# Kernel tuning notes

Hardware: AMD Instinct MI355X
Metric: run time of the kernel (lower is better)

The kernel has to match this reference:

```python
import jax, jax.numpy as jnp
import numpy as np

MAX_NODES = 1024
FEAT = 64
HID = 32
B, S = 32, 4096


def setup_inputs() -> dict:
    key = jax.random.key(0)
    ks = jax.random.split(key, 9)
    flow_features = jax.random.normal(ks[0], (B, S, FEAT), dtype=jnp.float32)
    src_ips = jax.random.randint(ks[1], (B, S), 0, MAX_NODES, dtype=jnp.int32)
    dst_ips = jax.random.randint(ks[2], (B, S), 0, MAX_NODES, dtype=jnp.int32)
    flow_volumes = jax.random.uniform(ks[3], (B, S), dtype=jnp.float32)
    # learned parameters
    node_emb = jax.random.normal(ks[4], (MAX_NODES, FEAT), dtype=jnp.float32)
    W1 = jax.random.normal(ks[5], (2 * FEAT, HID), dtype=jnp.float32) * (1.0 / np.sqrt(2 * FEAT))
    b1 = jnp.zeros((HID,), dtype=jnp.float32)
    W2 = jax.random.normal(ks[6], (HID, 1), dtype=jnp.float32) * (1.0 / np.sqrt(HID))
    b2 = jnp.zeros((1,), dtype=jnp.float32)
    return {"flow_features": flow_features, "src_ips": src_ips, "dst_ips": dst_ips,
            "flow_volumes": flow_volumes, "node_emb": node_emb,
            "W1": W1, "b1": b1, "W2": W2, "b2": b2}


def reference(flow_features, src_ips, dst_ips, flow_volumes, node_emb, W1, b1, W2, b2):
    b_, s_, f_ = flow_features.shape
    n_ = node_emb.shape[0]
    bidx = jnp.arange(b_)[:, None]  # (B,1) broadcast over seq

    # ---- scatter-add flow features into destination nodes ----
    node_features = jnp.zeros((b_, n_, f_), dtype=flow_features.dtype)
    node_features = node_features.at[bidx, dst_ips].add(flow_features)
    # F.normalize(p=2, dim=-1): x / max(||x||, eps)
    norm = jnp.linalg.norm(node_features, axis=-1, keepdims=True)
    node_features = node_features / jnp.maximum(norm, 1e-12)

    # ---- gather embeddings, edge MLP, scatter weights into adjacency ----
    src_e = node_emb[src_ips]  # (B,S,F)
    dst_e = node_emb[dst_ips]  # (B,S,F)
    h = jax.nn.relu(jnp.concatenate([src_e, dst_e], axis=-1) @ W1 + b1)  # (B,S,32)
    edge_w = jax.nn.sigmoid((h @ W2 + b2)[..., 0])  # (B,S)
    vol_w = jax.nn.sigmoid(flow_volumes / 1000.0)
    w = edge_w * vol_w  # (B,S)

    adjacency = jnp.zeros((b_, n_, n_), dtype=flow_features.dtype)
    # semantics up to scatter ordering of colliding edges)
    adjacency = adjacency.at[bidx, src_ips, dst_ips].set(w)
    adjacency = adjacency.at[bidx, dst_ips, src_ips].set(w)
    return node_features, adjacency
```

## Files before the change

kernel.cpp:

```cpp
#include <hip/hip_runtime.h>
#include <cstdint>
#include <cstddef>

#define BB 32
#define SS 4096
#define FEAT_ 64
#define HID_ 32
#define NN 1024

__global__ void node_feat_kernel(const float* __restrict__ flow,
                                 const int* __restrict__ dst,
                                 float* __restrict__ nf) {
    int row0 = blockIdx.x << 2;
    int b = row0 >> 10;
    __shared__ int sdst[SS];

    const int4* g = (const int4*)(dst + (size_t)b * SS);
    int4* sd4 = (int4*)sdst;
    for (int i = threadIdx.x; i < SS / 4; i += 256) sd4[i] = g[i];
    __syncthreads();

    int wave = threadIdx.x >> 6;
    int lane = threadIdx.x & 63;
    int node = (row0 + wave) & (NN - 1);
    const float* fb = flow + ((size_t)b * SS << 6);

    float acc = 0.0f;
    for (int s0 = 0; s0 < SS; s0 += 64) {
        int d = sdst[s0 + lane];
        unsigned long long m = __ballot(d == node);
        while (m) {
            int bit = __ffsll((long long)m) - 1;
            m &= m - 1;
            acc += fb[((s0 + bit) << 6) + lane];
        }
    }

    float ss = acc * acc;
    #pragma unroll
    for (int off = 32; off > 0; off >>= 1) ss += __shfl_xor(ss, off, 64);
    float denom = fmaxf(sqrtf(ss), 1e-12f);
    nf[((size_t)(row0 + wave) << 6) + lane] = acc / denom;
}

__global__ void scatter_prio_kernel(const int* __restrict__ src,
                                    const int* __restrict__ dst,
                                    float* __restrict__ adj) {
    int i = blockIdx.x * blockDim.x + threadIdx.x;
    int s = i & (SS - 1);
    int b = i >> 12;
    int si = src[i], di = dst[i];
    int* base = (int*)(adj + (size_t)b * NN * NN);
    atomicMax(base + si * NN + di, __float_as_int((float)(s + 1)));
    atomicMax(base + di * NN + si, __float_as_int((float)(SS + s + 1)));
}

__global__ void mlp_write_kernel(const int* __restrict__ src,
                                 const int* __restrict__ dst,
                                 const float* __restrict__ vol,
                                 const float* __restrict__ emb,
                                 const float* __restrict__ W1,
                                 const float* __restrict__ b1,
                                 const float* __restrict__ W2,
                                 const float* __restrict__ b2,
                                 float* __restrict__ adj) {
    int i = blockIdx.x * blockDim.x + threadIdx.x;
    int s = i & (SS - 1);
    int b = i >> 12;
    int si = src[i], di = dst[i];

    float acc[HID_];
    #pragma unroll
    for (int j = 0; j < HID_; ++j) acc[j] = b1[j];

    #pragma unroll
    for (int half = 0; half < 2; ++half) {
        const float* e = emb + ((half ? di : si) << 6);
        const float* w = W1 + half * 64 * HID_;
        for (int k = 0; k < 64; k += 4) {
            float4 v = *(const float4*)(e + k);
            #pragma unroll
            for (int j = 0; j < HID_; ++j) {
                float a = acc[j];
                a += v.x * w[(k + 0) * HID_ + j];
                a += v.y * w[(k + 1) * HID_ + j];
                a += v.z * w[(k + 2) * HID_ + j];
                a += v.w * w[(k + 3) * HID_ + j];
                acc[j] = a;
            }
        }
    }

    float dotv = b2[0];
    #pragma unroll
    for (int j = 0; j < HID_; ++j) dotv += fmaxf(acc[j], 0.0f) * W2[j];
    float edge_w = 1.0f / (1.0f + expf(-dotv));
    float vol_w  = 1.0f / (1.0f + expf(-vol[i] / 1000.0f));
    float wv = edge_w * vol_w;

    float* base = adj + (size_t)b * NN * NN;
    float* c1 = base + si * NN + di;
    float* c2 = base + di * NN + si;
    unsigned p1 = __float_as_uint((float)(s + 1));
    unsigned p2 = __float_as_uint((float)(SS + s + 1));
    if (__float_as_uint(*c1) == p1) *c1 = wv;
    if (__float_as_uint(*c2) == p2) *c2 = wv;
}

extern "C" void kernel_launch(void* const* d_in, const int* in_sizes, int n_in,
                              void* d_out, int out_size, void* d_ws, size_t ws_size,
                              hipStream_t stream) {
    const float* flow = (const float*)d_in[0];
    const int*   src  = (const int*)d_in[1];
    const int*   dst  = (const int*)d_in[2];
    const float* vol  = (const float*)d_in[3];
    const float* emb  = (const float*)d_in[4];
    const float* W1   = (const float*)d_in[5];
    const float* b1   = (const float*)d_in[6];
    const float* W2   = (const float*)d_in[7];
    const float* b2   = (const float*)d_in[8];

    float* nf  = (float*)d_out;
    float* adj = nf + (size_t)BB * NN * FEAT_;

    hipMemsetAsync(adj, 0, (size_t)BB * NN * NN * sizeof(float), stream);

    scatter_prio_kernel<<<(BB * SS) / 256, 256, 0, stream>>>(src, dst, adj);
    mlp_write_kernel<<<(BB * SS) / 256, 256, 0, stream>>>(src, dst, vol, emb,
                                                          W1, b1, W2, b2, adj);
    node_feat_kernel<<<(BB * NN) / 4, 256, 0, stream>>>(flow, dst, nf);
}
```

Measured before the change: 260.7 us.

## Build adjacency rows in shared memory instead of memset plus global atomics

Drops the full adjacency memset and the global atomicMax priority scatter. An MLP kernel now writes the edge weights to a workspace, and a row-block kernel builds each group of 16 adjacency rows in shared memory, resolving duplicate edges by a priority search. Each adjacency element is written exactly once with coalesced float4 stores. The cost is that every block rescans all 4096 edges of its batch, and each set cell does a linear search over the local edge list.

After: 1.006 ms. 286% more time.

```diff
diff --git a/kernel.cpp b/kernel.cpp
--- a/kernel.cpp
+++ b/kernel.cpp
@@ -7,6 +7,8 @@
 #define FEAT_ 64
 #define HID_ 32
 #define NN 1024
+#define RPB 16
+#define MAXL 1024
 
 __global__ void node_feat_kernel(const float* __restrict__ flow,
                                  const int* __restrict__ dst,
@@ -43,30 +45,16 @@
     nf[((size_t)(row0 + wave) << 6) + lane] = acc / denom;
 }
 
-__global__ void scatter_prio_kernel(const int* __restrict__ src,
-                                    const int* __restrict__ dst,
-                                    float* __restrict__ adj) {
+__global__ void mlp_kernel(const int* __restrict__ src,
+                           const int* __restrict__ dst,
+                           const float* __restrict__ vol,
+                           const float* __restrict__ emb,
+                           const float* __restrict__ W1,
+                           const float* __restrict__ b1,
+                           const float* __restrict__ W2,
+                           const float* __restrict__ b2,
+                           float* __restrict__ wout) {
     int i = blockIdx.x * blockDim.x + threadIdx.x;
-    int s = i & (SS - 1);
-    int b = i >> 12;
-    int si = src[i], di = dst[i];
-    int* base = (int*)(adj + (size_t)b * NN * NN);
-    atomicMax(base + si * NN + di, __float_as_int((float)(s + 1)));
-    atomicMax(base + di * NN + si, __float_as_int((float)(SS + s + 1)));
-}
-
-__global__ void mlp_write_kernel(const int* __restrict__ src,
-                                 const int* __restrict__ dst,
-                                 const float* __restrict__ vol,
-                                 const float* __restrict__ emb,
-                                 const float* __restrict__ W1,
-                                 const float* __restrict__ b1,
-                                 const float* __restrict__ W2,
-                                 const float* __restrict__ b2,
-                                 float* __restrict__ adj) {
-    int i = blockIdx.x * blockDim.x + threadIdx.x;
-    int s = i & (SS - 1);
-    int b = i >> 12;
     int si = src[i], di = dst[i];
 
     float acc[HID_];
@@ -96,15 +84,78 @@
     for (int j = 0; j < HID_; ++j) dotv += fmaxf(acc[j], 0.0f) * W2[j];
     float edge_w = 1.0f / (1.0f + expf(-dotv));
     float vol_w  = 1.0f / (1.0f + expf(-vol[i] / 1000.0f));
-    float wv = edge_w * vol_w;
+    wout[i] = edge_w * vol_w;
+}
 
-    float* base = adj + (size_t)b * NN * NN;
-    float* c1 = base + si * NN + di;
-    float* c2 = base + di * NN + si;
-    unsigned p1 = __float_as_uint((float)(s + 1));
-    unsigned p2 = __float_as_uint((float)(SS + s + 1));
-    if (__float_as_uint(*c1) == p1) *c1 = wv;
-    if (__float_as_uint(*c2) == p2) *c2 = wv;
+__global__ void adj_row_kernel(const int* __restrict__ src,
+                               const int* __restrict__ dst,
+                               const float* __restrict__ wbuf,
+                               float* __restrict__ adj) {
+    int b  = blockIdx.x >> 6;
+    int r0 = (blockIdx.x & 63) << 4;
+    int tid = threadIdx.x;
+
+    __shared__ int ssrc[SS];
+    __shared__ int sdst[SS];
+    __shared__ unsigned sbits[RPB][NN / 32];
+    __shared__ int lrc[MAXL];
+    __shared__ int lprio[MAXL];
+    __shared__ float lw[MAXL];
+    __shared__ int lcnt;
+
+    const int4* gs = (const int4*)(src + (size_t)b * SS);
+    const int4* gd = (const int4*)(dst + (size_t)b * SS);
+    int4* s4 = (int4*)ssrc;
+    int4* d4 = (int4*)sdst;
+    for (int i = tid; i < SS / 4; i += 256) { s4[i] = gs[i]; d4[i] = gd[i]; }
+    for (int i = tid; i < RPB * (NN / 32); i += 256) ((unsigned*)sbits)[i] = 0u;
+    if (tid == 0) lcnt = 0;
+    __syncthreads();
+
+    const float* wb = wbuf + (size_t)b * SS;
+    for (int s = tid; s < SS; s += 256) {
+        int sv = ssrc[s], dv = sdst[s];
+        unsigned lr1 = (unsigned)(sv - r0);
+        if (lr1 < RPB) {
+            int idx = atomicAdd(&lcnt, 1);
+            lrc[idx] = (int)((lr1 << 16) | (unsigned)dv);
+            lprio[idx] = s + 1;
+            lw[idx] = wb[s];
+            atomicOr(&sbits[lr1][dv >> 5], 1u << (dv & 31));
+        }
+        unsigned lr2 = (unsigned)(dv - r0);
+        if (lr2 < RPB) {
+            int idx = atomicAdd(&lcnt, 1);
+            lrc[idx] = (int)((lr2 << 16) | (unsigned)sv);
+            lprio[idx] = SS + s + 1;
+            lw[idx] = wb[s];
+            atomicOr(&sbits[lr2][sv >> 5], 1u << (sv & 31));
+        }
+    }
+    __syncthreads();
+
+    int cnt = lcnt;
+    for (int lr = 0; lr < RPB; ++lr) {
+        int colBase = tid << 2;
+        unsigned word = sbits[lr][tid >> 3];
+        unsigned bits = (word >> ((tid & 7) << 2)) & 0xFu;
+        float4 v = make_float4(0.f, 0.f, 0.f, 0.f);
+        if (bits) {
+            float* ve = &v.x;
+            #pragma unroll
+            for (int e = 0; e < 4; ++e) {
+                if (bits & (1u << e)) {
+                    int target = (lr << 16) | (colBase + e);
+                    int bp = -1; float bw = 0.f;
+                    for (int j = 0; j < cnt; ++j)
+                        if (lrc[j] == target && lprio[j] > bp) { bp = lprio[j]; bw = lw[j]; }
+                    ve[e] = bw;
+                }
+            }
+        }
+        float4* outrow = (float4*)(adj + ((size_t)b * NN + (r0 + lr)) * NN);
+        outrow[tid] = v;
+    }
 }
 
 extern "C" void kernel_launch(void* const* d_in, const int* in_sizes, int n_in,
@@ -122,11 +173,10 @@
 
     float* nf  = (float*)d_out;
     float* adj = nf + (size_t)BB * NN * FEAT_;
+    float* wbuf = (float*)d_ws;
 
-    hipMemsetAsync(adj, 0, (size_t)BB * NN * NN * sizeof(float), stream);
-
-    scatter_prio_kernel<<<(BB * SS) / 256, 256, 0, stream>>>(src, dst, adj);
-    mlp_write_kernel<<<(BB * SS) / 256, 256, 0, stream>>>(src, dst, vol, emb,
-                                                          W1, b1, W2, b2, adj);
+    mlp_kernel<<<(BB * SS) / 256, 256, 0, stream>>>(src, dst, vol, emb,
+                                                    W1, b1, W2, b2, wbuf);
+    adj_row_kernel<<<BB * (NN / RPB), 256, 0, stream>>>(src, dst, wbuf, adj);
     node_feat_kernel<<<(BB * NN) / 4, 256, 0, stream>>>(flow, dst, nf);
 }
```

## Build adjacency tiles in shared memory instead of memset plus global atomics

Applied to the files above, without the earlier changes.

Drops the full-size memset and the global atomicMax priority scatter. Edge weights are now computed into a workspace buffer, and a dense kernel builds each block's 8-row adjacency tile in LDS. Each block resolves last-write-wins with shared atomics, then writes the tile out with coalesced float4 stores. The cost is that every block rescans all 4096 edges of its batch, roughly 128x redundant index reads, in exchange for one streaming write pass over the adjacency.

After: 274.9 us. 1.05x slower.

```diff
diff --git a/kernel.cpp b/kernel.cpp
--- a/kernel.cpp
+++ b/kernel.cpp
@@ -7,6 +7,7 @@
 #define FEAT_ 64
 #define HID_ 32
 #define NN 1024
+#define RPB 8
 
 __global__ void node_feat_kernel(const float* __restrict__ flow,
                                  const int* __restrict__ dst,
@@ -43,30 +44,16 @@
     nf[((size_t)(row0 + wave) << 6) + lane] = acc / denom;
 }
 
-__global__ void scatter_prio_kernel(const int* __restrict__ src,
-                                    const int* __restrict__ dst,
-                                    float* __restrict__ adj) {
+__global__ void mlp_kernel(const int* __restrict__ src,
+                           const int* __restrict__ dst,
+                           const float* __restrict__ vol,
+                           const float* __restrict__ emb,
+                           const float* __restrict__ W1,
+                           const float* __restrict__ b1,
+                           const float* __restrict__ W2,
+                           const float* __restrict__ b2,
+                           float* __restrict__ wout) {
     int i = blockIdx.x * blockDim.x + threadIdx.x;
-    int s = i & (SS - 1);
-    int b = i >> 12;
-    int si = src[i], di = dst[i];
-    int* base = (int*)(adj + (size_t)b * NN * NN);
-    atomicMax(base + si * NN + di, __float_as_int((float)(s + 1)));
-    atomicMax(base + di * NN + si, __float_as_int((float)(SS + s + 1)));
-}
-
-__global__ void mlp_write_kernel(const int* __restrict__ src,
-                                 const int* __restrict__ dst,
-                                 const float* __restrict__ vol,
-                                 const float* __restrict__ emb,
-                                 const float* __restrict__ W1,
-                                 const float* __restrict__ b1,
-                                 const float* __restrict__ W2,
-                                 const float* __restrict__ b2,
-                                 float* __restrict__ adj) {
-    int i = blockIdx.x * blockDim.x + threadIdx.x;
-    int s = i & (SS - 1);
-    int b = i >> 12;
     int si = src[i], di = dst[i];
 
     float acc[HID_];
@@ -96,15 +83,56 @@
     for (int j = 0; j < HID_; ++j) dotv += fmaxf(acc[j], 0.0f) * W2[j];
     float edge_w = 1.0f / (1.0f + expf(-dotv));
     float vol_w  = 1.0f / (1.0f + expf(-vol[i] / 1000.0f));
-    float wv = edge_w * vol_w;
+    wout[i] = edge_w * vol_w;
+}
 
-    float* base = adj + (size_t)b * NN * NN;
-    float* c1 = base + si * NN + di;
-    float* c2 = base + di * NN + si;
-    unsigned p1 = __float_as_uint((float)(s + 1));
-    unsigned p2 = __float_as_uint((float)(SS + s + 1));
-    if (__float_as_uint(*c1) == p1) *c1 = wv;
-    if (__float_as_uint(*c2) == p2) *c2 = wv;
+__global__ void adj_dense_kernel(const int* __restrict__ src,
+                                 const int* __restrict__ dst,
+                                 const float* __restrict__ wbuf,
+                                 float* __restrict__ adj) {
+    int b  = blockIdx.x >> 7;
+    int r0 = (blockIdx.x & 127) << 3;
+    int tid = threadIdx.x;
+
+    __shared__ int D[RPB * NN];
+
+    int4* D4 = (int4*)D;
+    int4 z; z.x = z.y = z.z = z.w = 0;
+    #pragma unroll
+    for (int i = 0; i < RPB * NN / 4 / 256; ++i) D4[tid + i * 256] = z;
+    __syncthreads();
+
+    const int* sb = src + (size_t)b * SS;
+    const int* db = dst + (size_t)b * SS;
+
+    for (int s = tid; s < SS; s += 256) {
+        int sv = sb[s], dv = db[s];
+        unsigned lr1 = (unsigned)(sv - r0);
+        if (lr1 < RPB) atomicMax(&D[(lr1 << 10) + dv], s + 1);
+        unsigned lr2 = (unsigned)(dv - r0);
+        if (lr2 < RPB) atomicMax(&D[(lr2 << 10) + sv], SS + s + 1);
+    }
+    __syncthreads();
+
+    const float* wb = wbuf + (size_t)b * SS;
+    for (int s = tid; s < SS; s += 256) {
+        int sv = sb[s], dv = db[s];
+        unsigned lr1 = (unsigned)(sv - r0);
+        unsigned lr2 = (unsigned)(dv - r0);
+        if ((lr1 < RPB) | (lr2 < RPB)) {
+            int wbits = __float_as_int(wb[s]);
+            if (lr1 < RPB && D[(lr1 << 10) + dv] == s + 1)
+                D[(lr1 << 10) + dv] = wbits;
+            if (lr2 < RPB && D[(lr2 << 10) + sv] == SS + s + 1)
+                D[(lr2 << 10) + sv] = wbits;
+        }
+    }
+    __syncthreads();
+
+    const float4* Df = (const float4*)D;
+    float4* out = (float4*)(adj + ((size_t)b * NN + r0) * NN);
+    #pragma unroll
+    for (int i = 0; i < RPB * NN / 4 / 256; ++i) out[tid + i * 256] = Df[tid + i * 256];
 }
 
 extern "C" void kernel_launch(void* const* d_in, const int* in_sizes, int n_in,
@@ -122,11 +150,10 @@
 
     float* nf  = (float*)d_out;
     float* adj = nf + (size_t)BB * NN * FEAT_;
+    float* wbuf = (float*)d_ws;
 
-    hipMemsetAsync(adj, 0, (size_t)BB * NN * NN * sizeof(float), stream);
-
-    scatter_prio_kernel<<<(BB * SS) / 256, 256, 0, stream>>>(src, dst, adj);
-    mlp_write_kernel<<<(BB * SS) / 256, 256, 0, stream>>>(src, dst, vol, emb,
-                                                          W1, b1, W2, b2, adj);
+    mlp_kernel<<<(BB * SS) / 256, 256, 0, stream>>>(src, dst, vol, emb,
+                                                    W1, b1, W2, b2, wbuf);
+    adj_dense_kernel<<<BB * (NN / RPB), 256, 0, stream>>>(src, dst, wbuf, adj);
     node_feat_kernel<<<(BB * NN) / 4, 256, 0, stream>>>(flow, dst, nf);
 }
```
